# Optimization experiments

Hardware: AMD Instinct MI355X
Metric: run time of the kernel (lower is better)

## Reference

```python
import jax, jax.numpy as jnp
import numpy as np

H = 8  # LSTM units, from LSTM_Cell(8)
D = 32  # input feature dim
B = 256
T = 2048


def setup_inputs() -> dict:
    key = jax.random.key(0)
    k1, k2, k3 = jax.random.split(key, 3)
    x = jax.random.normal(k1, (B, T, D), dtype=jnp.float32)
    h0 = jnp.zeros((B, H), dtype=jnp.float32)
    c0 = jnp.zeros((B, H), dtype=jnp.float32)
    # standard LSTM cell params: gate order i, f, g (candidate), o
    Wx = jax.random.normal(k2, (D, 4 * H), dtype=jnp.float32) * (1.0 / np.sqrt(D))
    Wh = jax.random.normal(k3, (H, 4 * H), dtype=jnp.float32) * (1.0 / np.sqrt(H))
    b = jnp.zeros((4 * H,), dtype=jnp.float32)
    return {"x": x, "h0": h0, "c0": c0, "Wx": Wx, "Wh": Wh, "b": b}


def reference(x, h0, c0, Wx, Wh, b):
    """Unrolled LSTM recurrence over time, expressed as a fused lax.scan.

    Returns the per-timestep hidden states [B, T, H] (same math as the
    Python-loop layer, which collects h_t for every t) plus final (h, c).
    """
    xs = jnp.transpose(x, (1, 0, 2))  # [T, B, D]

    def step(carry, xt):
        h, c = carry
        z = xt @ Wx + h @ Wh + b  # [B, 4H]
        i, f, g, o = jnp.split(z, 4, axis=-1)
        i = jax.nn.sigmoid(i)
        f = jax.nn.sigmoid(f)
        g = jnp.tanh(g)
        o = jax.nn.sigmoid(o)
        c_new = f * c + i * g
        h_new = o * jnp.tanh(c_new)
        return (h_new, c_new), h_new

    (h_f, c_f), hs = jax.lax.scan(step, (h0, c0), xs)
    outputs = jnp.transpose(hs, (1, 0, 2))  # [B, T, H]
    return outputs, h_f, c_f
```

## Files before the change

kernel.cpp:

```cpp
#include <hip/hip_runtime.h>
#include <hip/hip_fp16.h>

#define T_STEPS 2048
#define BATCH   256

__device__ __forceinline__ float fexp2(float x) {
#if __has_builtin(__builtin_amdgcn_exp2f)
  return __builtin_amdgcn_exp2f(x);
#else
  return exp2f(x);
#endif
}
__device__ __forceinline__ float frcp(float x) {
#if __has_builtin(__builtin_amdgcn_rcpf)
  return __builtin_amdgcn_rcpf(x);
#else
  return 1.0f / x;
#endif
}

template<int CTRL>
__device__ __forceinline__ float dppf(float x) {
  int i = __float_as_int(x);
  int r = __builtin_amdgcn_update_dpp(i, i, CTRL, 0xF, 0xF, false);
  return __int_as_float(r);
}
#define DPP_X1   0xB1
#define DPP_X2   0x4E
#define DPP_MIR8 0x141

#define PIN(x) asm volatile("" : "+v"(x))

struct half4 { __half2 lo, hi; };

__global__ __launch_bounds__(256, 4) void zx_kernel(const float* __restrict__ x,
                                                    const float* __restrict__ Wx,
                                                    const float* __restrict__ bias,
                                                    unsigned* __restrict__ zx) {
  int wave = (blockIdx.x * 256 + (int)threadIdx.x) >> 6;
  int lane = (int)threadIdx.x & 63;
  int l    = lane & 31;
  int r    = lane >> 5;
  int j    = (l & 3) * 8 + (l >> 2);

  float wxc[32];
#pragma unroll
  for (int d = 0; d < 32; ++d) wxc[d] = Wx[d * 32 + j];
  float bj = bias[j];
#pragma unroll
  for (int d = 0; d < 32; ++d) PIN(wxc[d]);
  PIN(bj);

  int base = wave * 64;

  for (int it = 0; it < 32; ++it) {
    int row = base + (it << 1) + r;
    const float4* xr = (const float4*)(x + (size_t)row * 32);
    float a = bj, b2 = 0.0f;
#pragma unroll
    for (int qq = 0; qq < 8; ++qq) {
      float4 v = xr[qq];
      a  = fmaf(v.x, wxc[4*qq+0], a);
      b2 = fmaf(v.y, wxc[4*qq+1], b2);
      a  = fmaf(v.z, wxc[4*qq+2], a);
      b2 = fmaf(v.w, wxc[4*qq+3], b2);
    }
    float v  = a + b2;
    float pv = dppf<DPP_X1>(v);
    float lo = (l & 1) ? pv : v;
    float hi = (l & 1) ? v  : pv;
    union { _Float16 h2[2]; unsigned u; } pk;
    pk.h2[0] = (_Float16)lo;
    pk.h2[1] = (_Float16)hi;
    zx[(size_t)row * 16 + (l >> 1)] = pk.u;
  }
}

__global__ __launch_bounds__(64, 2) void lstm_kernel(const __half* __restrict__ zx,
                                                     const float* __restrict__ h0,
                                                     const float* __restrict__ c0,
                                                     const float* __restrict__ Wh,
                                                     float* __restrict__ out) {
  int lane = (int)threadIdx.x;
  int b = blockIdx.x * 8 + (lane >> 3);
  int s = lane & 7;

  constexpr int XM[8] = {0, 1, 2, 3, 7, 6, 5, 4};
  float wcf[8][4];
#pragma unroll
  for (int m = 0; m < 8; ++m) {
    int rowj = s ^ XM[m];
#pragma unroll
    for (int g = 0; g < 4; ++g) wcf[m][g] = Wh[rowj * 32 + g * 8 + s];
  }
#pragma unroll
  for (int m = 0; m < 8; ++m)
#pragma unroll
    for (int g = 0; g < 4; ++g) PIN(wcf[m][g]);

  float h = h0[b * 8 + s];
  float c = c0[b * 8 + s];

  const half4* zcur = (const half4*)zx + (size_t)b * T_STEPS * 8 + s;
  float*       ocur = out + (size_t)b * T_STEPS * 8 + s;

  constexpr int PD = 8;
  half4 buf[PD];
#pragma unroll
  for (int p = 0; p < PD; ++p) buf[p] = zcur[(size_t)p * 8];

#define STEP(pp, PREFETCH)                                                   \
  {                                                                          \
    float2 zif = __half22float2(buf[pp].lo);                                 \
    float2 zgo = __half22float2(buf[pp].hi);                                 \
    if (PREFETCH) buf[pp] = zcur[(pp + PD) * 8];                             \
    float r0 = h;                                                            \
    float r1 = dppf<DPP_X1>(r0);                                             \
    float r2 = dppf<DPP_X2>(r0);                                             \
    float r3 = dppf<DPP_X2>(r1);                                             \
    float r4 = dppf<DPP_MIR8>(r0);                                           \
    float r5 = dppf<DPP_MIR8>(r1);                                           \
    float r6 = dppf<DPP_MIR8>(r2);                                           \
    float r7 = dppf<DPP_MIR8>(r3);                                           \
    float rr[8] = {r0, r1, r2, r3, r4, r5, r6, r7};                          \
    float za[4] = {zif.x, zif.y, zgo.x, zgo.y};                              \
    float aA[4], aB[4];                                                      \
    _Pragma("unroll") for (int g = 0; g < 4; ++g) {                          \
      aA[g] = fmaf(rr[0], wcf[0][g], za[g]);                                 \
      aB[g] = rr[4] * wcf[4][g];                                             \
    }                                                                        \
    _Pragma("unroll") for (int m = 1; m < 4; ++m) {                          \
      _Pragma("unroll") for (int g = 0; g < 4; ++g) {                        \
        aA[g] = fmaf(rr[m],     wcf[m][g],     aA[g]);                       \
        aB[g] = fmaf(rr[m + 4], wcf[m + 4][g], aB[g]);                       \
      }                                                                      \
    }                                                                        \
    float iv = frcp(1.0f + fexp2(-1.442695040888963f * (aA[0] + aB[0])));    \
    float fv = frcp(1.0f + fexp2(-1.442695040888963f * (aA[1] + aB[1])));    \
    float gv = fmaf(2.0f, frcp(1.0f + fexp2(-2.885390081777927f *            \
                                            (aA[2] + aB[2]))), -1.0f);       \
    float ov = frcp(1.0f + fexp2(-1.442695040888963f * (aA[3] + aB[3])));    \
    c = fmaf(fv, c, iv * gv);                                                \
    float th = fmaf(2.0f, frcp(1.0f + fexp2(-2.885390081777927f * c)), -1.0f);\
    h = ov * th;                                                             \
    ocur[pp * 8] = h;                                                        \
  }

  for (int tb = 0; tb < T_STEPS - PD; tb += PD) {
    STEP(0, true) STEP(1, true) STEP(2, true) STEP(3, true)
    STEP(4, true) STEP(5, true) STEP(6, true) STEP(7, true)
    zcur += PD * 8;
    ocur += PD * 8;
  }
  STEP(0, false) STEP(1, false) STEP(2, false) STEP(3, false)
  STEP(4, false) STEP(5, false) STEP(6, false) STEP(7, false)
#undef STEP

  out[(size_t)BATCH * T_STEPS * 8 +             b * 8 + s] = h;
  out[(size_t)BATCH * T_STEPS * 8 + BATCH * 8 + b * 8 + s] = c;
}

extern "C" void kernel_launch(void* const* d_in, const int* in_sizes, int n_in,
                              void* d_out, int out_size, void* d_ws, size_t ws_size,
                              hipStream_t stream) {
  const float* x    = (const float*)d_in[0];
  const float* h0   = (const float*)d_in[1];
  const float* c0   = (const float*)d_in[2];
  const float* Wx   = (const float*)d_in[3];
  const float* Wh   = (const float*)d_in[4];
  const float* bias = (const float*)d_in[5];
  float* out = (float*)d_out;

  zx_kernel<<<2048, 256, 0, stream>>>(x, Wx, bias, (unsigned*)d_ws);
  lstm_kernel<<<BATCH / 8, 64, 0, stream>>>((const __half*)d_ws, h0, c0, Wh, out);
}
```

Baseline: 485.1 us.

## Split LSTM gates across lane pairs, doubling lanes per batch row

The recurrent kernel now uses 16 lanes per batch element instead of 8. Each lane pair splits the four gates two-and-two, so each lane does 16 FMAs and two transcendental activations per step instead of 32 FMAs and four, and gate results are exchanged with a DPP swap. The grid doubles to 64 blocks to cover the batch. Wx and Wh are staged through shared memory before being moved into registers, and the register pins move inside the loops. The serial per-step critical path gets shorter at the cost of an extra DPP exchange and select per step.

```diff
diff --git a/kernel.cpp b/kernel.cpp
--- a/kernel.cpp
+++ b/kernel.cpp
@@ -25,18 +25,28 @@
   int r = __builtin_amdgcn_update_dpp(i, i, CTRL, 0xF, 0xF, false);
   return __int_as_float(r);
 }
-#define DPP_X1   0xB1
-#define DPP_X2   0x4E
-#define DPP_MIR8 0x141
+#define DPP_X1 0xB1
+#define DPP_X2 0x4E
+#define DPP_HM 0x141
+#define DPP_RM 0x140
 
 #define PIN(x) asm volatile("" : "+v"(x))
 
-struct half4 { __half2 lo, hi; };
+#define L2E 1.442695040888963f
 
 __global__ __launch_bounds__(256, 4) void zx_kernel(const float* __restrict__ x,
                                                     const float* __restrict__ Wx,
                                                     const float* __restrict__ bias,
                                                     unsigned* __restrict__ zx) {
+  __shared__ float sWx[1024];
+  __shared__ float sb[32];
+  {
+    int t = (int)threadIdx.x;
+    for (int i = t; i < 1024; i += 256) sWx[i] = Wx[i];
+    if (t < 32) sb[t] = bias[t];
+  }
+  __syncthreads();
+
   int wave = (blockIdx.x * 256 + (int)threadIdx.x) >> 6;
   int lane = (int)threadIdx.x & 63;
   int l    = lane & 31;
@@ -45,15 +55,15 @@
 
   float wxc[32];
 #pragma unroll
-  for (int d = 0; d < 32; ++d) wxc[d] = Wx[d * 32 + j];
-  float bj = bias[j];
-#pragma unroll
-  for (int d = 0; d < 32; ++d) PIN(wxc[d]);
-  PIN(bj);
+  for (int d = 0; d < 32; ++d) wxc[d] = sWx[d * 32 + j];
+  float bj = sb[j];
 
   int base = wave * 64;
 
   for (int it = 0; it < 32; ++it) {
+#pragma unroll
+    for (int d = 0; d < 32; ++d) PIN(wxc[d]);
+    PIN(bj);
     int row = base + (it << 1) + r;
     const float4* xr = (const float4*)(x + (size_t)row * 32);
     float a = bj, b2 = 0.0f;
@@ -76,88 +86,97 @@
   }
 }
 
-__global__ __launch_bounds__(64, 2) void lstm_kernel(const __half* __restrict__ zx,
+__global__ __launch_bounds__(64, 1) void lstm_kernel(const __half* __restrict__ zx,
                                                      const float* __restrict__ h0,
                                                      const float* __restrict__ c0,
                                                      const float* __restrict__ Wh,
                                                      float* __restrict__ out) {
+  __shared__ float sWh[256];
   int lane = (int)threadIdx.x;
-  int b = blockIdx.x * 8 + (lane >> 3);
-  int s = lane & 7;
+  for (int i = lane; i < 256; i += 64) sWh[i] = Wh[i];
+  __syncthreads();
 
-  constexpr int XM[8] = {0, 1, 2, 3, 7, 6, 5, 4};
-  float wcf[8][4];
+  int b = blockIdx.x * 4 + (lane >> 4);
+  int q = lane & 15;
+  int u = q >> 1;
+  int p = q & 1;
+  bool pb = (p != 0);
+
+  float wA[8], wB[8];
 #pragma unroll
   for (int m = 0; m < 8; ++m) {
-    int rowj = s ^ XM[m];
-#pragma unroll
-    for (int g = 0; g < 4; ++g) wcf[m][g] = Wh[rowj * 32 + g * 8 + s];
+    int jrow = u ^ m;
+    wA[m] = sWh[jrow * 32 + (2 * p) * 8 + u];
+    wB[m] = sWh[jrow * 32 + (2 * p + 1) * 8 + u];
   }
-#pragma unroll
-  for (int m = 0; m < 8; ++m)
-#pragma unroll
-    for (int g = 0; g < 4; ++g) PIN(wcf[m][g]);
+  float cAc = pb ? -2.0f * L2E : -L2E;
+  float aAc = pb ? 2.0f : 1.0f;
+  float bAc = pb ? -1.0f : 0.0f;
 
-  float h = h0[b * 8 + s];
-  float c = c0[b * 8 + s];
+  float h = h0[b * 8 + u];
+  float c = c0[b * 8 + u];
 
-  const half4* zcur = (const half4*)zx + (size_t)b * T_STEPS * 8 + s;
-  float*       ocur = out + (size_t)b * T_STEPS * 8 + s;
+  const unsigned* zcur = (const unsigned*)zx + (size_t)b * T_STEPS * 16 + u * 2 + p;
+  float*          ocur = out + (size_t)b * T_STEPS * 8 + u;
 
   constexpr int PD = 8;
-  half4 buf[PD];
+  unsigned buf[PD];
 #pragma unroll
-  for (int p = 0; p < PD; ++p) buf[p] = zcur[(size_t)p * 8];
+  for (int pp = 0; pp < PD; ++pp) buf[pp] = zcur[pp * 16];
 
-#define STEP(pp, PREFETCH)                                                   \
+#define STEP(pp, PRE)                                                        \
   {                                                                          \
-    float2 zif = __half22float2(buf[pp].lo);                                 \
-    float2 zgo = __half22float2(buf[pp].hi);                                 \
-    if (PREFETCH) buf[pp] = zcur[(pp + PD) * 8];                             \
-    float r0 = h;                                                            \
-    float r1 = dppf<DPP_X1>(r0);                                             \
-    float r2 = dppf<DPP_X2>(r0);                                             \
-    float r3 = dppf<DPP_X2>(r1);                                             \
-    float r4 = dppf<DPP_MIR8>(r0);                                           \
-    float r5 = dppf<DPP_MIR8>(r1);                                           \
-    float r6 = dppf<DPP_MIR8>(r2);                                           \
-    float r7 = dppf<DPP_MIR8>(r3);                                           \
-    float rr[8] = {r0, r1, r2, r3, r4, r5, r6, r7};                          \
-    float za[4] = {zif.x, zif.y, zgo.x, zgo.y};                              \
-    float aA[4], aB[4];                                                      \
-    _Pragma("unroll") for (int g = 0; g < 4; ++g) {                          \
-      aA[g] = fmaf(rr[0], wcf[0][g], za[g]);                                 \
-      aB[g] = rr[4] * wcf[4][g];                                             \
-    }                                                                        \
-    _Pragma("unroll") for (int m = 1; m < 4; ++m) {                          \
-      _Pragma("unroll") for (int g = 0; g < 4; ++g) {                        \
-        aA[g] = fmaf(rr[m],     wcf[m][g],     aA[g]);                       \
-        aB[g] = fmaf(rr[m + 4], wcf[m + 4][g], aB[g]);                       \
-      }                                                                      \
-    }                                                                        \
-    float iv = frcp(1.0f + fexp2(-1.442695040888963f * (aA[0] + aB[0])));    \
-    float fv = frcp(1.0f + fexp2(-1.442695040888963f * (aA[1] + aB[1])));    \
-    float gv = fmaf(2.0f, frcp(1.0f + fexp2(-2.885390081777927f *            \
-                                            (aA[2] + aB[2]))), -1.0f);       \
-    float ov = frcp(1.0f + fexp2(-1.442695040888963f * (aA[3] + aB[3])));    \
+    union { unsigned u32; __half2 h2; } zz; zz.u32 = buf[pp];                \
+    float2 zf = __half22float2(zz.h2);         \
+    if (PRE) buf[pp] = zcur[(pp + PD) * 16];                                 \
+    float r0 = h;                                       \
+    float r1 = dppf<DPP_X2>(r0);                        \
+    float r3 = dppf<DPP_HM>(r0);                        \
+    float r7 = dppf<DPP_RM>(r0);                        \
+    float r2 = dppf<DPP_X2>(r3);                        \
+    float r6 = dppf<DPP_X2>(r7);                        \
+    float r4 = dppf<DPP_HM>(r7);                        \
+    float r5 = dppf<DPP_X2>(r4);                        \
+    float A0 = fmaf(r0, wA[0], zf.x);    \
+    float B0 = fmaf(r0, wB[0], zf.y);                                        \
+    float A1 = r1 * wA[1];                                                   \
+    float B1 = r1 * wB[1];                                                   \
+    A1 = fmaf(r3, wA[3], A1);  B1 = fmaf(r3, wB[3], B1);                     \
+    A0 = fmaf(r2, wA[2], A0);  B0 = fmaf(r2, wB[2], B0);                     \
+    A1 = fmaf(r7, wA[7], A1);  B1 = fmaf(r7, wB[7], B1);                     \
+    A0 = fmaf(r6, wA[6], A0);  B0 = fmaf(r6, wB[6], B0);                     \
+    A0 = fmaf(r4, wA[4], A0);  B0 = fmaf(r4, wB[4], B0);                     \
+    A1 = fmaf(r5, wA[5], A1);  B1 = fmaf(r5, wB[5], B1);                     \
+    float A = A0 + A1, B = B0 + B1;                                          \
+    float Aact = fmaf(aAc, frcp(1.0f + fexp2(cAc * A)), bAc);                \
+    float Bact = frcp(1.0f + fexp2(-L2E * B));                               \
+    float A2 = dppf<DPP_X1>(Aact);                                           \
+    float B2 = dppf<DPP_X1>(Bact);                                           \
+    float iv = pb ? A2   : Aact;                                             \
+    float fv = pb ? B2   : Bact;                                             \
+    float gv = pb ? Aact : A2;                                               \
+    float ov = pb ? Bact : B2;                                               \
     c = fmaf(fv, c, iv * gv);                                                \
-    float th = fmaf(2.0f, frcp(1.0f + fexp2(-2.885390081777927f * c)), -1.0f);\
+    float th = fmaf(2.0f, frcp(1.0f + fexp2(-2.0f * L2E * c)), -1.0f);       \
     h = ov * th;                                                             \
-    ocur[pp * 8] = h;                                                        \
+    ocur[pp * 8] = h;            \
   }
 
   for (int tb = 0; tb < T_STEPS - PD; tb += PD) {
-    STEP(0, true) STEP(1, true) STEP(2, true) STEP(3, true)
-    STEP(4, true) STEP(5, true) STEP(6, true) STEP(7, true)
-    zcur += PD * 8;
+#pragma unroll
+    for (int m = 0; m < 8; ++m) { PIN(wA[m]); PIN(wB[m]); }
+    PIN(cAc); PIN(aAc); PIN(bAc);
+    STEP(0, 1) STEP(1, 1) STEP(2, 1) STEP(3, 1)
+    STEP(4, 1) STEP(5, 1) STEP(6, 1) STEP(7, 1)
+    zcur += PD * 16;
     ocur += PD * 8;
   }
-  STEP(0, false) STEP(1, false) STEP(2, false) STEP(3, false)
-  STEP(4, false) STEP(5, false) STEP(6, false) STEP(7, false)
+  STEP(0, 0) STEP(1, 0) STEP(2, 0) STEP(3, 0)
+  STEP(4, 0) STEP(5, 0) STEP(6, 0) STEP(7, 0)
 #undef STEP
 
-  out[(size_t)BATCH * T_STEPS * 8 +             b * 8 + s] = h;
-  out[(size_t)BATCH * T_STEPS * 8 + BATCH * 8 + b * 8 + s] = c;
+  out[(size_t)BATCH * T_STEPS * 8 +             b * 8 + u] = h;
+  out[(size_t)BATCH * T_STEPS * 8 + BATCH * 8 + b * 8 + u] = c;
 }
 
 extern "C" void kernel_launch(void* const* d_in, const int* in_sizes, int n_in,
@@ -172,5 +191,5 @@
   float* out = (float*)d_out;
 
   zx_kernel<<<2048, 256, 0, stream>>>(x, Wx, bias, (unsigned*)d_ws);
-  lstm_kernel<<<BATCH / 8, 64, 0, stream>>>((const __half*)d_ws, h0, c0, Wh, out);
+  lstm_kernel<<<BATCH / 4, 64, 0, stream>>>((const __half*)d_ws, h0, c0, Wh, out);
 }
```

Result: faster. 421.0 us (-13.2%).
